# Kernel tuning notes

Hardware: AMD Instinct MI355X
Metric: run time of the kernel (lower is better)

The kernel has to match this reference:

```python
import jax, jax.numpy as jnp
import numpy as np

N = 100000      # nodes in first graph
D = 64          # latent_size
E1 = 3200000    # edges in graph 1
M = 200000      # link-nodes (rows of pos1)
E2 = 3200000    # edges in graph 2
P2 = 200000     # len(pos2), must be even
D1 = 2          # depth1
D2 = 2          # depth2
MAXX = 1000     # max_x


def _gcn(x, edge, W, b, n):
    row, col = edge[0], edge[1]
    xw = x @ W
    deg = jax.ops.segment_sum(jnp.ones(edge.shape[1], x.dtype), col, num_segments=n) + 1.0
    dinv = jax.lax.rsqrt(deg)
    msg = xw[row] * (dinv[row] * dinv[col])[:, None]
    agg = jax.ops.segment_sum(msg, col, num_segments=n) + xw * (dinv * dinv)[:, None]
    return agg + b


def _gn(x, w, b, ms):
    # PyG GraphNorm, single graph: (x - ms*mean)/sqrt(var+eps)*w + b
    mean = jnp.mean(x, axis=0, keepdims=True)
    c = x - ms * mean
    var = jnp.mean(c * c, axis=0, keepdims=True)
    return w * c * jax.lax.rsqrt(var + 1e-5) + b


def setup_inputs() -> dict:
    key = jax.random.key(0)
    ks = jax.random.split(key, 12)
    s = 0.1
    inp = {}
    inp["x"] = jax.random.randint(ks[0], (N,), 0, MAXX + 1)
    inp["na"] = jnp.zeros((1, 1), jnp.float32)  # unused (use_node_attr=False)
    inp["edge1"] = jax.random.randint(ks[1], (2, E1), 0, N)
    inp["edge2"] = jax.random.randint(ks[2], (2, E2), 0, M)
    inp["edge2_r"] = inp["edge2"][::-1]
    inp["pos1"] = jax.random.randint(ks[3], (M, 2), 0, N)
    inp["pos2"] = jax.random.randint(ks[4], (P2,), 0, M)
    inp["emb_table"] = jax.random.normal(ks[5], (MAXX + 1, D)) * s
    inp["emb_gn_w"] = jnp.ones((D,))
    inp["emb_gn_b"] = jnp.zeros((D,))
    inp["emb_gn_ms"] = jnp.ones((D,))

    def layer_params(k, depth):
        return (jax.random.normal(k, (depth, D, D)) * s,
                jnp.zeros((depth, D)),
                jnp.ones((depth, D)),
                jnp.zeros((depth, D)),
                jnp.ones((depth, D)))

    (inp["c1_W"], inp["c1_b"], inp["c1_gn_w"], inp["c1_gn_b"], inp["c1_gn_ms"]) = layer_params(ks[6], D1)
    (inp["c2_W"], inp["c2_b"], inp["c2_gn_w"], inp["c2_gn_b"], inp["c2_gn_ms"]) = layer_params(ks[7], D2)
    (inp["c2r_W"], inp["c2r_b"], inp["c2r_gn_w"], inp["c2r_gn_b"], inp["c2r_gn_ms"]) = layer_params(ks[8], D2)
    inp["pred_W"] = jax.random.normal(ks[9], (D, 1)) * s
    inp["pred_b"] = jnp.zeros((1,))
    return inp


def reference(x, na, edge1, edge2, edge2_r, pos1, pos2,
              emb_table, emb_gn_w, emb_gn_b, emb_gn_ms,
              c1_W, c1_b, c1_gn_w, c1_gn_b, c1_gn_ms,
              c2_W, c2_b, c2_gn_w, c2_gn_b, c2_gn_ms,
              c2r_W, c2r_b, c2r_gn_w, c2r_gn_b, c2r_gn_ms,
              pred_W, pred_b):
    # embedding + GraphNorm (dropout is identity at inference)
    h = emb_table[x]
    h = _gn(h, emb_gn_w, emb_gn_b, emb_gn_ms)
    # conv1 stack on the N-node graph
    for l in range(D1):
        h = jax.nn.relu(_gn(_gcn(h, edge1, c1_W[l], c1_b[l], N),
                            c1_gn_w[l], c1_gn_b[l], c1_gn_ms[l]))
    # pairwise gather-multiply -> M link-nodes
    h = h[pos1[:, 0]] * h[pos1[:, 1]]
    # dual-branch conv2 stack on the M-node graph
    for l in range(D2):
        a = jax.nn.relu(_gn(_gcn(h, edge2, c2_W[l], c2_b[l], M),
                            c2_gn_w[l], c2_gn_b[l], c2_gn_ms[l]))
        b2 = jax.nn.relu(_gn(_gcn(h, edge2_r, c2r_W[l], c2r_b[l], M),
                             c2r_gn_w[l], c2r_gn_b[l], c2r_gn_ms[l]))
        h = a + b2
    # pos2 gather, alternating mask == even/odd interleave, product, linear head
    h = h[pos2]
    h = h[0::2] * h[1::2]
    return h @ pred_W + pred_b
```

## Files before the change

kernel.cpp:

```cpp
#include <hip/hip_runtime.h>
#include <hip/hip_fp16.h>

#define NN 100000
#define MMn 200000
#define DD 64
#define NE1 3200000
#define NE2 3200000
#define SHB 6
#define NB1 1563
#define NB2 3125
#define CAP1 2560
#define CAP2 1536
#define NBLK 256
#define GGRID 2048

static inline int cdiv_l(long a, long b) { return (int)((a + b - 1) / b); }

__global__ void fill_i32_k(int* p, int v, long n) {
    long i = (long)blockIdx.x * blockDim.x + threadIdx.x;
    long st = (long)gridDim.x * blockDim.x;
    for (; i < n; i += st) p[i] = v;
}
__global__ void fill_f32_k(float* p, float v, long n) {
    long i = (long)blockIdx.x * blockDim.x + threadIdx.x;
    long st = (long)gridDim.x * blockDim.x;
    for (; i < n; i += st) p[i] = v;
}
__global__ void ginit_k(int* gcur, int nb, int cap) {
    int b = blockIdx.x * blockDim.x + threadIdx.x;
    if (b < nb) gcur[b] = b * cap;
}
__global__ void histx_k(const int* __restrict__ x, int n, int* __restrict__ freq) {
    int i = blockIdx.x * blockDim.x + threadIdx.x;
    if (i < n) atomicAdd(&freq[x[i]], 1);
}

__global__ __launch_bounds__(256) void stage_one_k(
    const int* __restrict__ keys, const int* __restrict__ vals, int ne,
    int* __restrict__ gcur, int2* __restrict__ stg, int nb, int cap)
{
    __shared__ int lcnt[3200];
    __shared__ int lbase[3200];
    int tid = threadIdx.x;
    for (int b = tid; b < nb; b += 256) lcnt[b] = 0;
    __syncthreads();
    int chunk = (ne + (int)gridDim.x - 1) / (int)gridDim.x;
    int s = blockIdx.x * chunk, e = min(ne, s + chunk);
    for (int i = s + tid; i < e; i += 256) atomicAdd(&lcnt[keys[i] >> SHB], 1);
    __syncthreads();
    for (int b = tid; b < nb; b += 256) {
        int c = lcnt[b];
        lbase[b] = c ? atomicAdd(&gcur[b], c) : 0;
        lcnt[b] = 0;
    }
    __syncthreads();
    for (int i = s + tid; i < e; i += 256) {
        int k = keys[i];
        int bkt = k >> SHB;
        int idx = atomicAdd(&lcnt[bkt], 1);
        long pos = (long)lbase[bkt] + idx;
        if (pos < (long)(bkt + 1) * cap) stg[pos] = make_int2(vals[i], k);
    }
}

template <int CAPT>
__global__ __launch_bounds__(256) void fill_one_k(
    const int2* __restrict__ stg, const int* __restrict__ gcur, int n,
    int* __restrict__ rows, int2* __restrict__ offs, float* __restrict__ dinv)
{
    __shared__ int2 ent[CAPT];
    __shared__ int deg[64];
    __shared__ int sstart[65];
    int b = blockIdx.x, tid = threadIdx.x;
    long s = (long)b * CAPT;
    int cnt = min(gcur[b] - (int)s, CAPT);
    if (tid < 64) deg[tid] = 0;
    __syncthreads();
    for (int i = tid; i < cnt; i += 256) {
        int2 u = stg[s + i];
        ent[i] = u;
        atomicAdd(&deg[u.y & 63], 1);
    }
    __syncthreads();
    if (tid == 0) {
        int acc = 0;
#pragma unroll
        for (int j = 0; j < 64; ++j) { sstart[j] = acc; acc += deg[j]; }
        sstart[64] = acc;
    }
    __syncthreads();
    int node = (b << SHB) + tid;
    if (tid < 64 && node < n) {
        int st = sstart[tid], en = sstart[tid + 1];
        offs[node] = make_int2((int)s + st, (int)s + en);
        dinv[node] = rsqrtf((float)(en - st) + 1.0f);
    }
    if (tid < 64) deg[tid] = sstart[tid];
    __syncthreads();
    for (int i = tid; i < cnt; i += 256) {
        int2 u = ent[i];
        int idx = atomicAdd(&deg[u.y & 63], 1);
        rows[s + idx] = u.x;
    }
}

__device__ __forceinline__ void gn_coef(const float* __restrict__ stats,
                                        const float* __restrict__ w, const float* __restrict__ b,
                                        const float* __restrict__ ms, float nrows, int d,
                                        float& sc, float& sh) {
    float mean = stats[d] / nrows;
    float ex2 = stats[64 + d] / nrows;
    float m = ms[d];
    float var = ex2 - mean * mean * (2.f * m - m * m);
    float is = rsqrtf(var + 1e-5f);
    sc = is * w[d];
    sh = b[d] - m * mean * sc;
}

__global__ __launch_bounds__(256) void tabstats_k(const float* __restrict__ T, const int* __restrict__ freq,
                                                  int nv, float* __restrict__ stats) {
    __shared__ float sS[256], sQ[256];
    int tid = threadIdx.x; int d = tid & 63; int g = tid >> 6;
    float s = 0.f, q = 0.f;
    for (int v = g; v < nv; v += 4) {
        float f = (float)freq[v];
        float t = T[(long)v * DD + d];
        s += f * t; q += f * t * t;
    }
    sS[tid] = s; sQ[tid] = q; __syncthreads();
    if (tid < 128) { sS[tid] += sS[tid + 128]; sQ[tid] += sQ[tid + 128]; }
    __syncthreads();
    if (tid < 64) { stats[d] = sS[tid] + sS[tid + 64]; stats[64 + d] = sQ[tid] + sQ[tid + 64]; }
}

__global__ void tnorm_k(const float* __restrict__ T, const float* __restrict__ stats,
                        const float* __restrict__ w, const float* __restrict__ b,
                        const float* __restrict__ ms, __half* __restrict__ Tn, int nv) {
    int i = blockIdx.x * blockDim.x + threadIdx.x;
    if (i >= nv * DD) return;
    int d = i & 63;
    float sc, sh;
    gn_coef(stats, w, b, ms, (float)NN, d, sc, sh);
    Tn[i] = __float2half(fmaf(T[i], sc, sh));
}

__device__ __forceinline__ void load_W4(const float* __restrict__ W, float4* sW4, int tid) {
    for (int idx = tid; idx < 1024; idx += 256) {
        int j = idx >> 6, dd = idx & 63;
        int k = j * 4;
        sW4[idx] = make_float4(W[k * 64 + dd], W[(k + 1) * 64 + dd],
                               W[(k + 2) * 64 + dd], W[(k + 3) * 64 + dd]);
    }
}

template <int NORM>
__global__ __launch_bounds__(256) void gcn_fused_k(
    const __half* __restrict__ hsrc, const int2* __restrict__ offs,
    const int* __restrict__ rows, const float* __restrict__ dinv,
    const float* __restrict__ stats, const float* __restrict__ gw,
    const float* __restrict__ gb, const float* __restrict__ gms, float nprev,
    const float* __restrict__ W, const float* __restrict__ bias,
    __half* __restrict__ Z, float* __restrict__ ostats, int n)
{
    __shared__ float4 sW4[1024];
    __shared__ float sP[256];
    __shared__ float rs[256];
    int tid = threadIdx.x;
    load_W4(W, sW4, tid);
    int wr = tid >> 6, d = tid & 63;
    int q = tid & 31, grp = (tid >> 5) & 1;
    int d0 = q * 2;
    float sc0 = 1.f, sh0 = 0.f, sc1 = 1.f, sh1 = 0.f;
    if (NORM) {
        gn_coef(stats, gw, gb, gms, nprev, d0, sc0, sh0);
        gn_coef(stats, gw, gb, gms, nprev, d0 + 1, sc1, sh1);
    }
    float bd = bias[d];
    float sumz = 0.f, sumq = 0.f;
    const __half2* h2 = (const __half2*)hsrc;
    float2* sPw = (float2*)(sP + wr * 64);
    const float4* sPv = (const float4*)(sP + wr * 64);
    int ngrp = (n + 3) >> 2;
    __syncthreads();
    for (int g = blockIdx.x; g < ngrp; g += gridDim.x) {
        int node = g * 4 + wr;
        if (node < n) {
            int2 se = offs[node];
            int s = se.x, e = se.y;
            float dc = dinv[node];
            float a0 = 0.f, a1 = 0.f, b0 = 0.f, b1 = 0.f;
            float c0 = 0.f, c1 = 0.f, e0 = 0.f, e1 = 0.f;
            if (!grp) {
                __half2 u = h2[(long)node * 32 + q];
                float x0 = __low2float(u), x1 = __high2float(u);
                if (NORM) {
                    x0 = fmaf(x0, sc0, sh0); x1 = fmaf(x1, sc1, sh1);
                    if (NORM == 2) { x0 = fmaxf(x0, 0.f); x1 = fmaxf(x1, 0.f); }
                }
                a0 = x0 * dc; a1 = x1 * dc;
            }
            int i = s + grp;
            for (; i + 6 < e; i += 8) {
                int r0 = rows[i], r1 = rows[i + 2], r2 = rows[i + 4], r3 = rows[i + 6];
                float w0 = dinv[r0], w1 = dinv[r1], w2 = dinv[r2], w3 = dinv[r3];
                __half2 u0 = h2[(long)r0 * 32 + q];
                __half2 u1 = h2[(long)r1 * 32 + q];
                __half2 u2 = h2[(long)r2 * 32 + q];
                __half2 u3 = h2[(long)r3 * 32 + q];
                float x00 = __low2float(u0), x01 = __high2float(u0);
                float x10 = __low2float(u1), x11 = __high2float(u1);
                float x20 = __low2float(u2), x21 = __high2float(u2);
                float x30 = __low2float(u3), x31 = __high2float(u3);
                if (NORM) {
                    x00 = fmaf(x00, sc0, sh0); x01 = fmaf(x01, sc1, sh1);
                    x10 = fmaf(x10, sc0, sh0); x11 = fmaf(x11, sc1, sh1);
                    x20 = fmaf(x20, sc0, sh0); x21 = fmaf(x21, sc1, sh1);
                    x30 = fmaf(x30, sc0, sh0); x31 = fmaf(x31, sc1, sh1);
                    if (NORM == 2) {
                        x00 = fmaxf(x00, 0.f); x01 = fmaxf(x01, 0.f);
                        x10 = fmaxf(x10, 0.f); x11 = fmaxf(x11, 0.f);
                        x20 = fmaxf(x20, 0.f); x21 = fmaxf(x21, 0.f);
                        x30 = fmaxf(x30, 0.f); x31 = fmaxf(x31, 0.f);
                    }
                }
                a0 = fmaf(x00, w0, a0); a1 = fmaf(x01, w0, a1);
                b0 = fmaf(x10, w1, b0); b1 = fmaf(x11, w1, b1);
                c0 = fmaf(x20, w2, c0); c1 = fmaf(x21, w2, c1);
                e0 = fmaf(x30, w3, e0); e1 = fmaf(x31, w3, e1);
            }
            for (; i < e; i += 2) {
                int r = rows[i];
                float w0 = dinv[r];
                __half2 u = h2[(long)r * 32 + q];
                float x0 = __low2float(u), x1 = __high2float(u);
                if (NORM) {
                    x0 = fmaf(x0, sc0, sh0); x1 = fmaf(x1, sc1, sh1);
                    if (NORM == 2) { x0 = fmaxf(x0, 0.f); x1 = fmaxf(x1, 0.f); }
                }
                a0 = fmaf(x0, w0, a0); a1 = fmaf(x1, w0, a1);
            }
            a0 = (a0 + b0) + (c0 + e0);
            a1 = (a1 + b1) + (c1 + e1);
            a0 += __shfl_xor(a0, 32, 64);
            a1 += __shfl_xor(a1, 32, 64);
            if (!grp) sPw[q] = make_float2(a0 * dc, a1 * dc);
            float z = bd;
#pragma unroll
            for (int j = 0; j < 16; ++j) {
                float4 pv = sPv[j];
                float4 wv = sW4[j * 64 + d];
                z = fmaf(pv.x, wv.x, z); z = fmaf(pv.y, wv.y, z);
                z = fmaf(pv.z, wv.z, z); z = fmaf(pv.w, wv.w, z);
            }
            Z[(long)node * DD + d] = __float2half(z);
            sumz += z; sumq += z * z;
        }
    }
    __syncthreads();
    rs[tid] = sumz; __syncthreads();
    if (tid < 64) atomicAdd(&ostats[tid], rs[tid] + rs[tid + 64] + rs[tid + 128] + rs[tid + 192]);
    __syncthreads();
    rs[tid] = sumq; __syncthreads();
    if (tid < 64) atomicAdd(&ostats[64 + tid], rs[tid] + rs[tid + 64] + rs[tid + 128] + rs[tid + 192]);
}

__global__ __launch_bounds__(256) void gcn_tab_fused_k(
    const __half* __restrict__ Tn, const int* __restrict__ xidx,
    const int2* __restrict__ offs, const int* __restrict__ rows,
    const float* __restrict__ dinv,
    const float* __restrict__ W, const float* __restrict__ bias,
    __half* __restrict__ Z, float* __restrict__ ostats, int n)
{
    __shared__ float4 sW4[1024];
    __shared__ float sP[256];
    __shared__ float rs[256];
    int tid = threadIdx.x;
    load_W4(W, sW4, tid);
    int wr = tid >> 6, d = tid & 63;
    int q = tid & 31, grp = (tid >> 5) & 1;
    float bd = bias[d];
    float sumz = 0.f, sumq = 0.f;
    const __half2* t2 = (const __half2*)Tn;
    float2* sPw = (float2*)(sP + wr * 64);
    const float4* sPv = (const float4*)(sP + wr * 64);
    int ngrp = (n + 3) >> 2;
    __syncthreads();
    for (int g = blockIdx.x; g < ngrp; g += gridDim.x) {
        int node = g * 4 + wr;
        if (node < n) {
            int2 se = offs[node];
            int s = se.x, e = se.y;
            float dc = dinv[node];
            float a0 = 0.f, a1 = 0.f, b0 = 0.f, b1 = 0.f;
            float c0 = 0.f, c1 = 0.f, e0 = 0.f, e1 = 0.f;
            if (!grp) {
                __half2 u = t2[(long)xidx[node] * 32 + q];
                a0 = __low2float(u) * dc; a1 = __high2float(u) * dc;
            }
            int i = s + grp;
            for (; i + 6 < e; i += 8) {
                int r0 = rows[i], r1 = rows[i + 2], r2 = rows[i + 4], r3 = rows[i + 6];
                float w0 = dinv[r0], w1 = dinv[r1], w2 = dinv[r2], w3 = dinv[r3];
                __half2 u0 = t2[(long)xidx[r0] * 32 + q];
                __half2 u1 = t2[(long)xidx[r1] * 32 + q];
                __half2 u2 = t2[(long)xidx[r2] * 32 + q];
                __half2 u3 = t2[(long)xidx[r3] * 32 + q];
                a0 = fmaf(__low2float(u0), w0, a0); a1 = fmaf(__high2float(u0), w0, a1);
                b0 = fmaf(__low2float(u1), w1, b0); b1 = fmaf(__high2float(u1), w1, b1);
                c0 = fmaf(__low2float(u2), w2, c0); c1 = fmaf(__high2float(u2), w2, c1);
                e0 = fmaf(__low2float(u3), w3, e0); e1 = fmaf(__high2float(u3), w3, e1);
            }
            for (; i < e; i += 2) {
                int r = rows[i];
                float w0 = dinv[r];
                __half2 u = t2[(long)xidx[r] * 32 + q];
                a0 = fmaf(__low2float(u), w0, a0); a1 = fmaf(__high2float(u), w0, a1);
            }
            a0 = (a0 + b0) + (c0 + e0);
            a1 = (a1 + b1) + (c1 + e1);
            a0 += __shfl_xor(a0, 32, 64);
            a1 += __shfl_xor(a1, 32, 64);
            if (!grp) sPw[q] = make_float2(a0 * dc, a1 * dc);
            float z = bd;
#pragma unroll
            for (int j = 0; j < 16; ++j) {
                float4 pv = sPv[j];
                float4 wv = sW4[j * 64 + d];
                z = fmaf(pv.x, wv.x, z); z = fmaf(pv.y, wv.y, z);
                z = fmaf(pv.z, wv.z, z); z = fmaf(pv.w, wv.w, z);
            }
            Z[(long)node * DD + d] = __float2half(z);
            sumz += z; sumq += z * z;
        }
    }
    __syncthreads();
    rs[tid] = sumz; __syncthreads();
    if (tid < 64) atomicAdd(&ostats[tid], rs[tid] + rs[tid + 64] + rs[tid + 128] + rs[tid + 192]);
    __syncthreads();
    rs[tid] = sumq; __syncthreads();
    if (tid < 64) atomicAdd(&ostats[64 + tid], rs[tid] + rs[tid + 64] + rs[tid + 128] + rs[tid + 192]);
}

__global__ __launch_bounds__(256) void pair_norm_mul_k(
    const __half* __restrict__ Z2, const int* __restrict__ pos,
    const float* __restrict__ stats, const float* __restrict__ gw,
    const float* __restrict__ gb, const float* __restrict__ gms,
    __half* __restrict__ h2)
{
    int tid = threadIdx.x, wr = tid >> 6, d = tid & 63;
    int idx = blockIdx.x * 4 + wr;
    if (idx >= MMn) return;
    float sc, sh;
    gn_coef(stats, gw, gb, gms, (float)NN, d, sc, sh);
    int p0 = pos[2 * idx], p1 = pos[2 * idx + 1];
    float v0 = fmaxf(fmaf(__half2float(Z2[(long)p0 * DD + d]), sc, sh), 0.f);
    float v1 = fmaxf(fmaf(__half2float(Z2[(long)p1 * DD + d]), sc, sh), 0.f);
    h2[(long)idx * DD + d] = __float2half(v0 * v1);
}

__global__ __launch_bounds__(256) void dualadd_k(
    const __half2* __restrict__ Za, const __half2* __restrict__ Zb,
    const float* __restrict__ stA, const float* __restrict__ wA, const float* __restrict__ bA, const float* __restrict__ msA,
    const float* __restrict__ stB, const float* __restrict__ wB, const float* __restrict__ bB, const float* __restrict__ msB,
    __half2* __restrict__ hout)
{
    const long nu = (long)MMn * 32;
    int tid = threadIdx.x;
    int d0 = (2 * tid) & 63;
    float scA0, shA0, scA1, shA1, scB0, shB0, scB1, shB1;
    gn_coef(stA, wA, bA, msA, (float)MMn, d0, scA0, shA0);
    gn_coef(stA, wA, bA, msA, (float)MMn, d0 + 1, scA1, shA1);
    gn_coef(stB, wB, bB, msB, (float)MMn, d0, scB0, shB0);
    gn_coef(stB, wB, bB, msB, (float)MMn, d0 + 1, scB1, shB1);
    for (long i = (long)blockIdx.x * 256 + tid; i < nu; i += (long)gridDim.x * 256) {
        __half2 ua = Za[i], ub = Zb[i];
        float a0 = __low2float(ua), a1 = __high2float(ua);
        float c0 = __low2float(ub), c1 = __high2float(ub);
        float o0 = fmaxf(fmaf(a0, scA0, shA0), 0.f) + fmaxf(fmaf(c0, scB0, shB0), 0.f);
        float o1 = fmaxf(fmaf(a1, scA1, shA1), 0.f) + fmaxf(fmaf(c1, scB1, shB1), 0.f);
        hout[i] = __halves2half2(__float2half(o0), __float2half(o1));
    }
}

__global__ __launch_bounds__(256) void final_fused_k(
    const __half* __restrict__ Za, const __half* __restrict__ Zb,
    const int* __restrict__ pos2,
    const float* __restrict__ stA, const float* __restrict__ wA, const float* __restrict__ bA, const float* __restrict__ msA,
    const float* __restrict__ stB, const float* __restrict__ wB, const float* __restrict__ bB, const float* __restrict__ msB,
    const float* __restrict__ pw, const float* __restrict__ pb,
    float* __restrict__ out, int nout)
{
    int tid = threadIdx.x, wr = tid >> 6, d = tid & 63;
    int i = blockIdx.x * 4 + wr;
    if (i >= nout) return;
    float scA, shA, scB, shB;
    gn_coef(stA, wA, bA, msA, (float)MMn, d, scA, shA);
    gn_coef(stB, wB, bB, msB, (float)MMn, d, scB, shB);
    int p0 = pos2[2 * i], p1 = pos2[2 * i + 1];
    float v0 = fmaxf(fmaf(__half2float(Za[(long)p0 * DD + d]), scA, shA), 0.f)
             + fmaxf(fmaf(__half2float(Zb[(long)p0 * DD + d]), scB, shB), 0.f);
    float v1 = fmaxf(fmaf(__half2float(Za[(long)p1 * DD + d]), scA, shA), 0.f)
             + fmaxf(fmaf(__half2float(Zb[(long)p1 * DD + d]), scB, shB), 0.f);
    float v = v0 * v1 * pw[d];
#pragma unroll
    for (int o = 32; o > 0; o >>= 1) v += __shfl_down(v, o, 64);
    if (d == 0) out[i] = v + pb[0];
}

extern "C" void kernel_launch(void* const* d_in, const int* in_sizes, int n_in,
                              void* d_out, int out_size, void* d_ws, size_t ws_size,
                              hipStream_t stream) {
    const int* x      = (const int*)d_in[0];
    const int* edge1  = (const int*)d_in[2];
    const int* edge2  = (const int*)d_in[3];
    const int* pos1   = (const int*)d_in[5];
    const int* pos2   = (const int*)d_in[6];
    const float* emb  = (const float*)d_in[7];
    const float* egw  = (const float*)d_in[8];
    const float* egb  = (const float*)d_in[9];
    const float* egm  = (const float*)d_in[10];
    const float* c1W  = (const float*)d_in[11];
    const float* c1b  = (const float*)d_in[12];
    const float* c1gw = (const float*)d_in[13];
    const float* c1gb = (const float*)d_in[14];
    const float* c1gm = (const float*)d_in[15];
    const float* c2W  = (const float*)d_in[16];
    const float* c2b  = (const float*)d_in[17];
    const float* c2gw = (const float*)d_in[18];
    const float* c2gb = (const float*)d_in[19];
    const float* c2gm = (const float*)d_in[20];
    const float* c2rW  = (const float*)d_in[21];
    const float* c2rb  = (const float*)d_in[22];
    const float* c2rgw = (const float*)d_in[23];
    const float* c2rgb = (const float*)d_in[24];
    const float* c2rgm = (const float*)d_in[25];
    const float* predW = (const float*)d_in[26];
    const float* predb = (const float*)d_in[27];
    float* out = (float*)d_out;
    const int NV = 1001;

    char* p = (char*)d_ws;
    const long SZH = (long)MMn * DD;
    __half* BA = (__half*)p; p += SZH * 2;
    __half* BB = (__half*)p; p += SZH * 2;
    __half* BC = (__half*)p; p += SZH * 2;
    int2* stg  = (int2*)p;  p += (long)NB2 * CAP2 * 8;
    int* rows1 = (int*)p; p += (long)NB1 * CAP1 * 4;
    int* rowsA = (int*)p; p += (long)NB2 * CAP2 * 4;
    int* rowsB = (int*)p; p += (long)NB2 * CAP2 * 4;
    int2* offs1 = (int2*)p; p += (long)NN * 8;
    int2* offsA = (int2*)p; p += (long)MMn * 8;
    int2* offsB = (int2*)p; p += (long)MMn * 8;
    float* dinv1  = (float*)p; p += (long)NN * 4;
    float* dinv2  = (float*)p; p += (long)MMn * 4;
    float* dinv2r = (float*)p; p += (long)MMn * 4;
    int* gcur1 = (int*)p; p += 2048 * 4;
    int* gcurA = (int*)p; p += 4096 * 4;
    int* gcurB = (int*)p; p += 4096 * 4;
    int* freq = (int*)p; p += 1024 * 4;
    float* stats = (float*)p; p += 7 * 128 * 4;
    __half* Tn = (__half*)p; p += (long)NV * DD * 2;
    if ((size_t)(p - (char*)d_ws) > ws_size) return;

    fill_i32_k<<<4, 256, 0, stream>>>(freq, 0, 1024);
    fill_f32_k<<<1, 256, 0, stream>>>(stats, 0.f, 7 * 128);

    histx_k<<<cdiv_l(NN, 256), 256, 0, stream>>>(x, NN, freq);
    tabstats_k<<<1, 256, 0, stream>>>(emb, freq, NV, stats);
    tnorm_k<<<cdiv_l((long)NV * DD, 256), 256, 0, stream>>>(emb, stats, egw, egb, egm, Tn, NV);

    ginit_k<<<cdiv_l(NB1, 256), 256, 0, stream>>>(gcur1, NB1, CAP1);
    stage_one_k<<<NBLK, 256, 0, stream>>>(edge1 + NE1, edge1, NE1, gcur1, stg, NB1, CAP1);
    fill_one_k<CAP1><<<NB1, 256, 0, stream>>>(stg, gcur1, NN, rows1, offs1, dinv1);

    ginit_k<<<cdiv_l(NB2, 256), 256, 0, stream>>>(gcurA, NB2, CAP2);
    stage_one_k<<<NBLK, 256, 0, stream>>>(edge2 + NE2, edge2, NE2, gcurA, stg, NB2, CAP2);
    fill_one_k<CAP2><<<NB2, 256, 0, stream>>>(stg, gcurA, MMn, rowsA, offsA, dinv2);

    ginit_k<<<cdiv_l(NB2, 256), 256, 0, stream>>>(gcurB, NB2, CAP2);
    stage_one_k<<<NBLK, 256, 0, stream>>>(edge2, edge2 + NE2, NE2, gcurB, stg, NB2, CAP2);
    fill_one_k<CAP2><<<NB2, 256, 0, stream>>>(stg, gcurB, MMn, rowsB, offsB, dinv2r);

    gcn_tab_fused_k<<<GGRID, 256, 0, stream>>>(Tn, x, offs1, rows1, dinv1, c1W, c1b, BB, stats + 128, NN);

    gcn_fused_k<2><<<GGRID, 256, 0, stream>>>(BB, offs1, rows1, dinv1,
        stats + 128, c1gw, c1gb, c1gm, (float)NN, c1W + 4096, c1b + 64, BA, stats + 256, NN);

    pair_norm_mul_k<<<cdiv_l(MMn, 4), 256, 0, stream>>>(BA, pos1,
        stats + 256, c1gw + 64, c1gb + 64, c1gm + 64, BC);

    gcn_fused_k<0><<<GGRID, 256, 0, stream>>>(BC, offsA, rowsA, dinv2,
        stats, nullptr, nullptr, nullptr, 1.f, c2W, c2b, BB, stats + 384, MMn);
    gcn_fused_k<0><<<GGRID, 256, 0, stream>>>(BC, offsB, rowsB, dinv2r,
        stats, nullptr, nullptr, nullptr, 1.f, c2rW, c2rb, BA, stats + 512, MMn);
    dualadd_k<<<1024, 256, 0, stream>>>((const __half2*)BB, (const __half2*)BA,
        stats + 384, c2gw, c2gb, c2gm,
        stats + 512, c2rgw, c2rgb, c2rgm, (__half2*)BC);

    gcn_fused_k<0><<<GGRID, 256, 0, stream>>>(BC, offsA, rowsA, dinv2,
        stats, nullptr, nullptr, nullptr, 1.f, c2W + 4096, c2b + 64, BB, stats + 640, MMn);
    gcn_fused_k<0><<<GGRID, 256, 0, stream>>>(BC, offsB, rowsB, dinv2r,
        stats, nullptr, nullptr, nullptr, 1.f, c2rW + 4096, c2rb + 64, BA, stats + 768, MMn);

    final_fused_k<<<cdiv_l(out_size, 4), 256, 0, stream>>>(BB, BA, pos2,
        stats + 640, c2gw + 64, c2gb + 64, c2gm + 64,
        stats + 768, c2rgw + 64, c2rgb + 64, c2rgm + 64,
        predW, predb, out, out_size);
}
```

Before: 1.431 ms.

## Prescale conv2 inputs by source dinv and pack staged edges into one int

```diff
diff --git a/kernel.cpp b/kernel.cpp
--- a/kernel.cpp
+++ b/kernel.cpp
@@ -37,7 +37,7 @@
 
 __global__ __launch_bounds__(256) void stage_one_k(
     const int* __restrict__ keys, const int* __restrict__ vals, int ne,
-    int* __restrict__ gcur, int2* __restrict__ stg, int nb, int cap)
+    int* __restrict__ gcur, int* __restrict__ stg, int nb, int cap)
 {
     __shared__ int lcnt[3200];
     __shared__ int lbase[3200];
@@ -59,16 +59,16 @@
         int bkt = k >> SHB;
         int idx = atomicAdd(&lcnt[bkt], 1);
         long pos = (long)lbase[bkt] + idx;
-        if (pos < (long)(bkt + 1) * cap) stg[pos] = make_int2(vals[i], k);
+        if (pos < (long)(bkt + 1) * cap) stg[pos] = (vals[i] << 6) | (k & 63);
     }
 }
 
 template <int CAPT>
 __global__ __launch_bounds__(256) void fill_one_k(
-    const int2* __restrict__ stg, const int* __restrict__ gcur, int n,
+    const int* __restrict__ stg, const int* __restrict__ gcur, int n,
     int* __restrict__ rows, int2* __restrict__ offs, float* __restrict__ dinv)
 {
-    __shared__ int2 ent[CAPT];
+    __shared__ int ent[CAPT];
     __shared__ int deg[64];
     __shared__ int sstart[65];
     int b = blockIdx.x, tid = threadIdx.x;
@@ -77,9 +77,9 @@
     if (tid < 64) deg[tid] = 0;
     __syncthreads();
     for (int i = tid; i < cnt; i += 256) {
-        int2 u = stg[s + i];
+        int u = stg[s + i];
         ent[i] = u;
-        atomicAdd(&deg[u.y & 63], 1);
+        atomicAdd(&deg[u & 63], 1);
     }
     __syncthreads();
     if (tid == 0) {
@@ -98,9 +98,9 @@
     if (tid < 64) deg[tid] = sstart[tid];
     __syncthreads();
     for (int i = tid; i < cnt; i += 256) {
-        int2 u = ent[i];
-        int idx = atomicAdd(&deg[u.y & 63], 1);
-        rows[s + idx] = u.x;
+        int u = ent[i];
+        int idx = atomicAdd(&deg[u & 63], 1);
+        rows[s + idx] = ((unsigned)u) >> 6;
     }
 }
 
@@ -153,12 +153,9 @@
     }
 }
 
-template <int NORM>
-__global__ __launch_bounds__(256) void gcn_fused_k(
+__global__ __launch_bounds__(256) void gcn_sum_k(
     const __half* __restrict__ hsrc, const int2* __restrict__ offs,
     const int* __restrict__ rows, const float* __restrict__ dinv,
-    const float* __restrict__ stats, const float* __restrict__ gw,
-    const float* __restrict__ gb, const float* __restrict__ gms, float nprev,
     const float* __restrict__ W, const float* __restrict__ bias,
     __half* __restrict__ Z, float* __restrict__ ostats, int n)
 {
@@ -169,12 +166,6 @@
     load_W4(W, sW4, tid);
     int wr = tid >> 6, d = tid & 63;
     int q = tid & 31, grp = (tid >> 5) & 1;
-    int d0 = q * 2;
-    float sc0 = 1.f, sh0 = 0.f, sc1 = 1.f, sh1 = 0.f;
-    if (NORM) {
-        gn_coef(stats, gw, gb, gms, nprev, d0, sc0, sh0);
-        gn_coef(stats, gw, gb, gms, nprev, d0 + 1, sc1, sh1);
-    }
     float bd = bias[d];
     float sumz = 0.f, sumq = 0.f;
     const __half2* h2 = (const __half2*)hsrc;
@@ -192,11 +183,96 @@
             float c0 = 0.f, c1 = 0.f, e0 = 0.f, e1 = 0.f;
             if (!grp) {
                 __half2 u = h2[(long)node * 32 + q];
-                float x0 = __low2float(u), x1 = __high2float(u);
-                if (NORM) {
-                    x0 = fmaf(x0, sc0, sh0); x1 = fmaf(x1, sc1, sh1);
-                    if (NORM == 2) { x0 = fmaxf(x0, 0.f); x1 = fmaxf(x1, 0.f); }
-                }
+                a0 = __low2float(u); a1 = __high2float(u);
+            }
+            int i = s + grp;
+            for (; i + 14 < e; i += 16) {
+                int r0 = rows[i],      r1 = rows[i + 2],  r2 = rows[i + 4],  r3 = rows[i + 6];
+                int r4 = rows[i + 8],  r5 = rows[i + 10], r6 = rows[i + 12], r7 = rows[i + 14];
+                __half2 u0 = h2[(long)r0 * 32 + q];
+                __half2 u1 = h2[(long)r1 * 32 + q];
+                __half2 u2 = h2[(long)r2 * 32 + q];
+                __half2 u3 = h2[(long)r3 * 32 + q];
+                __half2 u4 = h2[(long)r4 * 32 + q];
+                __half2 u5 = h2[(long)r5 * 32 + q];
+                __half2 u6 = h2[(long)r6 * 32 + q];
+                __half2 u7 = h2[(long)r7 * 32 + q];
+                a0 += __low2float(u0); a1 += __high2float(u0);
+                b0 += __low2float(u1); b1 += __high2float(u1);
+                c0 += __low2float(u2); c1 += __high2float(u2);
+                e0 += __low2float(u3); e1 += __high2float(u3);
+                a0 += __low2float(u4); a1 += __high2float(u4);
+                b0 += __low2float(u5); b1 += __high2float(u5);
+                c0 += __low2float(u6); c1 += __high2float(u6);
+                e0 += __low2float(u7); e1 += __high2float(u7);
+            }
+            for (; i < e; i += 2) {
+                __half2 u = h2[(long)rows[i] * 32 + q];
+                a0 += __low2float(u); a1 += __high2float(u);
+            }
+            a0 = (a0 + b0) + (c0 + e0);
+            a1 = (a1 + b1) + (c1 + e1);
+            a0 += __shfl_xor(a0, 32, 64);
+            a1 += __shfl_xor(a1, 32, 64);
+            if (!grp) sPw[q] = make_float2(a0 * dc, a1 * dc);
+            float z = bd;
+#pragma unroll
+            for (int j = 0; j < 16; ++j) {
+                float4 pv = sPv[j];
+                float4 wv = sW4[j * 64 + d];
+                z = fmaf(pv.x, wv.x, z); z = fmaf(pv.y, wv.y, z);
+                z = fmaf(pv.z, wv.z, z); z = fmaf(pv.w, wv.w, z);
+            }
+            Z[(long)node * DD + d] = __float2half(z);
+            sumz += z; sumq += z * z;
+        }
+    }
+    __syncthreads();
+    rs[tid] = sumz; __syncthreads();
+    if (tid < 64) atomicAdd(&ostats[tid], rs[tid] + rs[tid + 64] + rs[tid + 128] + rs[tid + 192]);
+    __syncthreads();
+    rs[tid] = sumq; __syncthreads();
+    if (tid < 64) atomicAdd(&ostats[64 + tid], rs[tid] + rs[tid + 64] + rs[tid + 128] + rs[tid + 192]);
+}
+
+__global__ __launch_bounds__(256) void gcn_fused_k(
+    const __half* __restrict__ hsrc, const int2* __restrict__ offs,
+    const int* __restrict__ rows, const float* __restrict__ dinv,
+    const float* __restrict__ stats, const float* __restrict__ gw,
+    const float* __restrict__ gb, const float* __restrict__ gms, float nprev,
+    const float* __restrict__ W, const float* __restrict__ bias,
+    __half* __restrict__ Z, float* __restrict__ ostats, int n)
+{
+    __shared__ float4 sW4[1024];
+    __shared__ float sP[256];
+    __shared__ float rs[256];
+    int tid = threadIdx.x;
+    load_W4(W, sW4, tid);
+    int wr = tid >> 6, d = tid & 63;
+    int q = tid & 31, grp = (tid >> 5) & 1;
+    int d0 = q * 2;
+    float sc0, sh0, sc1, sh1;
+    gn_coef(stats, gw, gb, gms, nprev, d0, sc0, sh0);
+    gn_coef(stats, gw, gb, gms, nprev, d0 + 1, sc1, sh1);
+    float bd = bias[d];
+    float sumz = 0.f, sumq = 0.f;
+    const __half2* h2 = (const __half2*)hsrc;
+    float2* sPw = (float2*)(sP + wr * 64);
+    const float4* sPv = (const float4*)(sP + wr * 64);
+    int ngrp = (n + 3) >> 2;
+    __syncthreads();
+    for (int g = blockIdx.x; g < ngrp; g += gridDim.x) {
+        int node = g * 4 + wr;
+        if (node < n) {
+            int2 se = offs[node];
+            int s = se.x, e = se.y;
+            float dc = dinv[node];
+            float a0 = 0.f, a1 = 0.f, b0 = 0.f, b1 = 0.f;
+            float c0 = 0.f, c1 = 0.f, e0 = 0.f, e1 = 0.f;
+            if (!grp) {
+                __half2 u = h2[(long)node * 32 + q];
+                float x0 = fmaxf(fmaf(__low2float(u), sc0, sh0), 0.f);
+                float x1 = fmaxf(fmaf(__high2float(u), sc1, sh1), 0.f);
                 a0 = x0 * dc; a1 = x1 * dc;
             }
             int i = s + grp;
@@ -207,22 +283,14 @@
                 __half2 u1 = h2[(long)r1 * 32 + q];
                 __half2 u2 = h2[(long)r2 * 32 + q];
                 __half2 u3 = h2[(long)r3 * 32 + q];
-                float x00 = __low2float(u0), x01 = __high2float(u0);
-                float x10 = __low2float(u1), x11 = __high2float(u1);
-                float x20 = __low2float(u2), x21 = __high2float(u2);
-                float x30 = __low2float(u3), x31 = __high2float(u3);
-                if (NORM) {
-                    x00 = fmaf(x00, sc0, sh0); x01 = fmaf(x01, sc1, sh1);
-                    x10 = fmaf(x10, sc0, sh0); x11 = fmaf(x11, sc1, sh1);
-                    x20 = fmaf(x20, sc0, sh0); x21 = fmaf(x21, sc1, sh1);
-                    x30 = fmaf(x30, sc0, sh0); x31 = fmaf(x31, sc1, sh1);
-                    if (NORM == 2) {
-                        x00 = fmaxf(x00, 0.f); x01 = fmaxf(x01, 0.f);
-                        x10 = fmaxf(x10, 0.f); x11 = fmaxf(x11, 0.f);
-                        x20 = fmaxf(x20, 0.f); x21 = fmaxf(x21, 0.f);
-                        x30 = fmaxf(x30, 0.f); x31 = fmaxf(x31, 0.f);
-                    }
-                }
+                float x00 = fmaxf(fmaf(__low2float(u0), sc0, sh0), 0.f);
+                float x01 = fmaxf(fmaf(__high2float(u0), sc1, sh1), 0.f);
+                float x10 = fmaxf(fmaf(__low2float(u1), sc0, sh0), 0.f);
+                float x11 = fmaxf(fmaf(__high2float(u1), sc1, sh1), 0.f);
+                float x20 = fmaxf(fmaf(__low2float(u2), sc0, sh0), 0.f);
+                float x21 = fmaxf(fmaf(__high2float(u2), sc1, sh1), 0.f);
+                float x30 = fmaxf(fmaf(__low2float(u3), sc0, sh0), 0.f);
+                float x31 = fmaxf(fmaf(__high2float(u3), sc1, sh1), 0.f);
                 a0 = fmaf(x00, w0, a0); a1 = fmaf(x01, w0, a1);
                 b0 = fmaf(x10, w1, b0); b1 = fmaf(x11, w1, b1);
                 c0 = fmaf(x20, w2, c0); c1 = fmaf(x21, w2, c1);
@@ -232,11 +300,8 @@
                 int r = rows[i];
                 float w0 = dinv[r];
                 __half2 u = h2[(long)r * 32 + q];
-                float x0 = __low2float(u), x1 = __high2float(u);
-                if (NORM) {
-                    x0 = fmaf(x0, sc0, sh0); x1 = fmaf(x1, sc1, sh1);
-                    if (NORM == 2) { x0 = fmaxf(x0, 0.f); x1 = fmaxf(x1, 0.f); }
-                }
+                float x0 = fmaxf(fmaf(__low2float(u), sc0, sh0), 0.f);
+                float x1 = fmaxf(fmaf(__high2float(u), sc1, sh1), 0.f);
                 a0 = fmaf(x0, w0, a0); a1 = fmaf(x1, w0, a1);
             }
             a0 = (a0 + b0) + (c0 + e0);
@@ -345,7 +410,8 @@
     const __half* __restrict__ Z2, const int* __restrict__ pos,
     const float* __restrict__ stats, const float* __restrict__ gw,
     const float* __restrict__ gb, const float* __restrict__ gms,
-    __half* __restrict__ h2)
+    const float* __restrict__ dinvA, const float* __restrict__ dinvB,
+    __half* __restrict__ ha, __half* __restrict__ hb)
 {
     int tid = threadIdx.x, wr = tid >> 6, d = tid & 63;
     int idx = blockIdx.x * 4 + wr;
@@ -355,14 +421,17 @@
     int p0 = pos[2 * idx], p1 = pos[2 * idx + 1];
     float v0 = fmaxf(fmaf(__half2float(Z2[(long)p0 * DD + d]), sc, sh), 0.f);
     float v1 = fmaxf(fmaf(__half2float(Z2[(long)p1 * DD + d]), sc, sh), 0.f);
-    h2[(long)idx * DD + d] = __float2half(v0 * v1);
+    float v = v0 * v1;
+    ha[(long)idx * DD + d] = __float2half(v * dinvA[idx]);
+    hb[(long)idx * DD + d] = __float2half(v * dinvB[idx]);
 }
 
 __global__ __launch_bounds__(256) void dualadd_k(
     const __half2* __restrict__ Za, const __half2* __restrict__ Zb,
     const float* __restrict__ stA, const float* __restrict__ wA, const float* __restrict__ bA, const float* __restrict__ msA,
     const float* __restrict__ stB, const float* __restrict__ wB, const float* __restrict__ bB, const float* __restrict__ msB,
-    __half2* __restrict__ hout)
+    const float* __restrict__ dinvA, const float* __restrict__ dinvB,
+    __half2* __restrict__ ha, __half2* __restrict__ hb)
 {
     const long nu = (long)MMn * 32;
     int tid = threadIdx.x;
@@ -378,7 +447,10 @@
         float c0 = __low2float(ub), c1 = __high2float(ub);
         float o0 = fmaxf(fmaf(a0, scA0, shA0), 0.f) + fmaxf(fmaf(c0, scB0, shB0), 0.f);
         float o1 = fmaxf(fmaf(a1, scA1, shA1), 0.f) + fmaxf(fmaf(c1, scB1, shB1), 0.f);
-        hout[i] = __halves2half2(__float2half(o0), __float2half(o1));
+        int node = (int)(i >> 5);
+        float wa = dinvA[node], wb = dinvB[node];
+        ha[i] = __halves2half2(__float2half(o0 * wa), __float2half(o1 * wa));
+        hb[i] = __halves2half2(__float2half(o0 * wb), __float2half(o1 * wb));
     }
 }
 
@@ -444,7 +516,8 @@
     __half* BA = (__half*)p; p += SZH * 2;
     __half* BB = (__half*)p; p += SZH * 2;
     __half* BC = (__half*)p; p += SZH * 2;
-    int2* stg  = (int2*)p;  p += (long)NB2 * CAP2 * 8;
+    __half* BD = (__half*)p; p += SZH * 2;
+    int* stg   = (int*)p;   p += (long)NB2 * CAP2 * 4;
     int* rows1 = (int*)p; p += (long)NB1 * CAP1 * 4;
     int* rowsA = (int*)p; p += (long)NB2 * CAP2 * 4;
     int* rowsB = (int*)p; p += (long)NB2 * CAP2 * 4;
@@ -483,24 +556,21 @@
 
     gcn_tab_fused_k<<<GGRID, 256, 0, stream>>>(Tn, x, offs1, rows1, dinv1, c1W, c1b, BB, stats + 128, NN);
 
-    gcn_fused_k<2><<<GGRID, 256, 0, stream>>>(BB, offs1, rows1, dinv1,
+    gcn_fused_k<<<GGRID, 256, 0, stream>>>(BB, offs1, rows1, dinv1,
         stats + 128, c1gw, c1gb, c1gm, (float)NN, c1W + 4096, c1b + 64, BA, stats + 256, NN);
 
     pair_norm_mul_k<<<cdiv_l(MMn, 4), 256, 0, stream>>>(BA, pos1,
-        stats + 256, c1gw + 64, c1gb + 64, c1gm + 64, BC);
-
-    gcn_fused_k<0><<<GGRID, 256, 0, stream>>>(BC, offsA, rowsA, dinv2,
-        stats, nullptr, nullptr, nullptr, 1.f, c2W, c2b, BB, stats + 384, MMn);
-    gcn_fused_k<0><<<GGRID, 256, 0, stream>>>(BC, offsB, rowsB, dinv2r,
-        stats, nullptr, nullptr, nullptr, 1.f, c2rW, c2rb, BA, stats + 512, MMn);
+        stats + 256, c1gw + 64, c1gb + 64, c1gm + 64, dinv2, dinv2r, BC, BD);
+
+    gcn_sum_k<<<GGRID, 256, 0, stream>>>(BC, offsA, rowsA, dinv2, c2W, c2b, BB, stats + 384, MMn);
+    gcn_sum_k<<<GGRID, 256, 0, stream>>>(BD, offsB, rowsB, dinv2r, c2rW, c2rb, BA, stats + 512, MMn);
     dualadd_k<<<1024, 256, 0, stream>>>((const __half2*)BB, (const __half2*)BA,
         stats + 384, c2gw, c2gb, c2gm,
-        stats + 512, c2rgw, c2rgb, c2rgm, (__half2*)BC);
-
-    gcn_fused_k<0><<<GGRID, 256, 0, stream>>>(BC, offsA, rowsA, dinv2,
-        stats, nullptr, nullptr, nullptr, 1.f, c2W + 4096, c2b + 64, BB, stats + 640, MMn);
-    gcn_fused_k<0><<<GGRID, 256, 0, stream>>>(BC, offsB, rowsB, dinv2r,
-        stats, nullptr, nullptr, nullptr, 1.f, c2rW + 4096, c2rb + 64, BA, stats + 768, MMn);
+        stats + 512, c2rgw, c2rgb, c2rgm,
+        dinv2, dinv2r, (__half2*)BC, (__half2*)BD);
+
+    gcn_sum_k<<<GGRID, 256, 0, stream>>>(BC, offsA, rowsA, dinv2, c2W + 4096, c2b + 64, BB, stats + 640, MMn);
+    gcn_sum_k<<<GGRID, 256, 0, stream>>>(BD, offsB, rowsB, dinv2r, c2rW + 4096, c2rb + 64, BA, stats + 768, MMn);
 
     final_fused_k<<<cdiv_l(out_size, 4), 256, 0, stream>>>(BB, BA, pos2,
         stats + 640, c2gw + 64, c2gb + 64, c2gm + 64,
```

New measurement: 1.481 ms. 3.5% more time.
